# Performance work log

Hardware: AMD Instinct MI355X
Metric: run time of the kernel (lower is better)

Reference implementation:

```python
import jax, jax.numpy as jnp
import numpy as np

# Quantization constants (from Conv2D.set_fixed_point / set_zero_points)
Q_MANTISSA = 1305500416  # int32 fixed-point multiplier mantissa
EXPONENT = -7            # fixed-point exponent
OUT_ZP = -5              # output zero point
KH, KW, KD = 3, 3, 1     # filter window (filter shape [F, 3, 3, 1])


def setup_inputs() -> dict:
    key = jax.random.key(0)
    k1, k2, k3 = jax.random.split(key, 3)
    F, H, W, D = 64, 514, 514, 4
    x = jax.random.randint(k1, (F, H, W, D), -128, 128, dtype=jnp.int32).astype(jnp.int8)
    w = jax.random.randint(k2, (F, KH, KW, KD), -128, 128, dtype=jnp.int32).astype(jnp.int8)
    b = jax.random.randint(k3, (F,), -1000, 1000, dtype=jnp.int32)
    return {"x": x, "w": w, "b": b}


def reference(x, w, b):
    # x: int8 [F, H, W, D]; w: int8 [F, 3, 3, 1]; b: int32 [F]
    F, H, W, D = x.shape
    OH, OW, OD = H - (KH - 1), W - (KW - 1), D - (KD - 1)
    # Grouped valid correlation: out[i,j,k,l] = sum_{m,n,o} x[i,j+m,k+n,l+o]*w[i,m,n,o]
    acc = jnp.zeros((F, OH, OW, OD), dtype=jnp.int32)
    for m in range(KH):
        for n in range(KW):
            for o in range(KD):
                acc = acc + (x[:, m:m + OH, n:n + OW, o:o + OD].astype(jnp.int32)
                             * w[:, m, n, o].astype(jnp.int32)[:, None, None, None])
    acc = acc + b[:, None, None, None]
    # multiply_by_quantize_mul: note python precedence -> (q_mantissa + (1<<15)) >> 16
    if Q_MANTISSA < 2147418112:
        reduced_mantissa = (Q_MANTISSA + (1 << 15)) >> 16
    else:
        reduced_mantissa = 32767
    total_shifts = 15 - EXPONENT
    x64 = acc.astype(jnp.int64) * jnp.int64(reduced_mantissa)
    x64 = x64 + jnp.int64(1 << (total_shifts - 1))
    res = jnp.right_shift(x64, total_shifts)  # arithmetic shift (signed)
    out = jnp.clip(res + OUT_ZP, -128, 127).astype(jnp.int8)
    return out
```

## Files before the change

kernel.cpp:

```cpp
#include <hip/hip_runtime.h>


#define NF 64
#define HH 514
#define WW 514
#define OH 512
#define OW 512
#define RB 4

__device__ __forceinline__ int quantize(int acc) {
    long long t = (long long)acc * 19920LL + (1LL << 21);
    int r = (int)(t >> 22) - 5;
    r = max(-128, min(127, r));
    return r;
}

__global__ __launch_bounds__(256) void conv2d_q_kernel(const int* __restrict__ x,
                                                       const int* __restrict__ w,
                                                       const int* __restrict__ b,
                                                       int* __restrict__ out) {
    const int f   = blockIdx.z;
    const int oh0 = blockIdx.y * RB;
    const int ow  = blockIdx.x * 256 + threadIdx.x;

    int wgt[9];
#pragma unroll
    for (int k = 0; k < 9; ++k) wgt[k] = w[f * 9 + k];
    const int bias = b[f];

    const int4* __restrict__ xv = reinterpret_cast<const int4*>(x);
    int4* __restrict__ ov = reinterpret_cast<int4*>(out);

    int acc[RB][4];
#pragma unroll
    for (int r = 0; r < RB; ++r)
#pragma unroll
        for (int c = 0; c < 4; ++c) acc[r][c] = bias;

    const int xbase = (f * HH + oh0) * WW + ow;

#pragma unroll
    for (int h = 0; h < RB + 2; ++h) {
        const int4 t0 = xv[xbase + h * WW + 0];
        const int4 t1 = xv[xbase + h * WW + 1];
        const int4 t2 = xv[xbase + h * WW + 2];
#pragma unroll
        for (int r = 0; r < RB; ++r) {
            const int m = h - r;
            if (m >= 0 && m < 3) {
                const int c0 = wgt[m * 3 + 0];
                const int c1 = wgt[m * 3 + 1];
                const int c2 = wgt[m * 3 + 2];
                acc[r][0] += t0.x * c0 + t1.x * c1 + t2.x * c2;
                acc[r][1] += t0.y * c0 + t1.y * c1 + t2.y * c2;
                acc[r][2] += t0.z * c0 + t1.z * c1 + t2.z * c2;
                acc[r][3] += t0.w * c0 + t1.w * c1 + t2.w * c2;
            }
        }
    }

    const int obase = (f * OH + oh0) * OW + ow;
#pragma unroll
    for (int r = 0; r < RB; ++r) {
        int4 o;
        o.x = quantize(acc[r][0]);
        o.y = quantize(acc[r][1]);
        o.z = quantize(acc[r][2]);
        o.w = quantize(acc[r][3]);
        ov[obase + r * OW] = o;
    }
}

extern "C" void kernel_launch(void* const* d_in, const int* in_sizes, int n_in,
                              void* d_out, int out_size, void* d_ws, size_t ws_size,
                              hipStream_t stream) {
    const int* x = (const int*)d_in[0];
    const int* w = (const int*)d_in[1];
    const int* b = (const int*)d_in[2];
    int* out = (int*)d_out;

    dim3 grid(OW / 256, OH / RB, NF);
    dim3 block(256, 1, 1);
    conv2d_q_kernel<<<grid, block, 0, stream>>>(x, w, b, out);
}
```

Baseline: 435.9 us.

## Double row tile, swizzle workgroups across XCDs, use nontemporal stores

Increases output rows per thread from 4 to 8 to cut redundant halo row loads. Flattens the grid and remaps workgroup IDs so consecutive IDs on each XCD cover contiguous regions, improving L2 locality. Replaces the 64-bit quantize multiply with an equivalent 32-bit form and writes outputs with nontemporal stores to avoid polluting cache. Higher RB raises register use and halves workgroup count.

Result: slower. 445.1 us (+2.1%).

```diff
diff --git a/kernel.cpp b/kernel.cpp
--- a/kernel.cpp
+++ b/kernel.cpp
@@ -1,35 +1,39 @@
 #include <hip/hip_runtime.h>
 
+
+typedef int v4i __attribute__((ext_vector_type(4)));
 
 #define NF 64
 #define HH 514
 #define WW 514
 #define OH 512
 #define OW 512
-#define RB 4
+#define RB 8
+#define NWG (2 * (OH / RB) * NF)
 
 __device__ __forceinline__ int quantize(int acc) {
-    long long t = (long long)acc * 19920LL + (1LL << 21);
-    int r = (int)(t >> 22) - 5;
-    r = max(-128, min(127, r));
-    return r;
+    int r = ((acc * 4980 + (1 << 19)) >> 20) - 5;
+    return max(-128, min(127, r));
 }
 
 __global__ __launch_bounds__(256) void conv2d_q_kernel(const int* __restrict__ x,
                                                        const int* __restrict__ w,
                                                        const int* __restrict__ b,
                                                        int* __restrict__ out) {
-    const int f   = blockIdx.z;
-    const int oh0 = blockIdx.y * RB;
-    const int ow  = blockIdx.x * 256 + threadIdx.x;
+    const int wg  = blockIdx.x;
+    const int swz = (wg & 7) * (NWG / 8) + (wg >> 3);
+    const int f   = swz >> 7;
+    const int rem = swz & 127;
+    const int oh0 = (rem >> 1) * RB;
+    const int ow  = (rem & 1) * 256 + threadIdx.x;
 
     int wgt[9];
 #pragma unroll
     for (int k = 0; k < 9; ++k) wgt[k] = w[f * 9 + k];
     const int bias = b[f];
 
-    const int4* __restrict__ xv = reinterpret_cast<const int4*>(x);
-    int4* __restrict__ ov = reinterpret_cast<int4*>(out);
+    const v4i* __restrict__ xv = reinterpret_cast<const v4i*>(x);
+    v4i* __restrict__ ov = reinterpret_cast<v4i*>(out);
 
     int acc[RB][4];
 #pragma unroll
@@ -41,9 +45,9 @@
 
 #pragma unroll
     for (int h = 0; h < RB + 2; ++h) {
-        const int4 t0 = xv[xbase + h * WW + 0];
-        const int4 t1 = xv[xbase + h * WW + 1];
-        const int4 t2 = xv[xbase + h * WW + 2];
+        const v4i t0 = xv[xbase + h * WW + 0];
+        const v4i t1 = xv[xbase + h * WW + 1];
+        const v4i t2 = xv[xbase + h * WW + 2];
 #pragma unroll
         for (int r = 0; r < RB; ++r) {
             const int m = h - r;
@@ -51,10 +55,9 @@
                 const int c0 = wgt[m * 3 + 0];
                 const int c1 = wgt[m * 3 + 1];
                 const int c2 = wgt[m * 3 + 2];
-                acc[r][0] += t0.x * c0 + t1.x * c1 + t2.x * c2;
-                acc[r][1] += t0.y * c0 + t1.y * c1 + t2.y * c2;
-                acc[r][2] += t0.z * c0 + t1.z * c1 + t2.z * c2;
-                acc[r][3] += t0.w * c0 + t1.w * c1 + t2.w * c2;
+#pragma unroll
+                for (int c = 0; c < 4; ++c)
+                    acc[r][c] += t0[c] * c0 + t1[c] * c1 + t2[c] * c2;
             }
         }
     }
@@ -62,12 +65,10 @@
     const int obase = (f * OH + oh0) * OW + ow;
 #pragma unroll
     for (int r = 0; r < RB; ++r) {
-        int4 o;
-        o.x = quantize(acc[r][0]);
-        o.y = quantize(acc[r][1]);
-        o.z = quantize(acc[r][2]);
-        o.w = quantize(acc[r][3]);
-        ov[obase + r * OW] = o;
+        v4i o;
+#pragma unroll
+        for (int c = 0; c < 4; ++c) o[c] = quantize(acc[r][c]);
+        __builtin_nontemporal_store(o, &ov[obase + r * OW]);
     }
 }
 
@@ -79,7 +80,7 @@
     const int* b = (const int*)d_in[2];
     int* out = (int*)d_out;
 
-    dim3 grid(OW / 256, OH / RB, NF);
+    dim3 grid(NWG, 1, 1);
     dim3 block(256, 1, 1);
     conv2d_q_kernel<<<grid, block, 0, stream>>>(x, w, b, out);
 }
```
